# Kernel optimization log

Hardware: AMD Instinct MI355X
Metric: run time of the kernel (lower is better)

Reference implementation:

```python
import jax, jax.numpy as jnp
import numpy as np

N_M, N_C, D, H, E, EL = 200000, 50000, 128, 64, 1000000, 100000


def gat_conv(h_src, h_dst, W_src, W_dst, a_src, a_dst, b, src, dst, n_dst):
    # PyG GATConv (heads=1): project, per-edge attention logit, segment softmax over dst, weighted scatter-sum.
    hs = h_src @ W_src                      # [Ns, H]
    hd = h_dst @ W_dst                      # [Nd, H]
    al_s = hs @ a_src                       # [Ns]
    al_d = hd @ a_dst                       # [Nd]
    alpha = jax.nn.leaky_relu(al_s[src] + al_d[dst], 0.2)   # [E]
    m = jax.ops.segment_max(alpha, dst, num_segments=n_dst)
    m = jnp.where(jnp.isfinite(m), m, 0.0)
    e = jnp.exp(alpha - m[dst])
    denom = jax.ops.segment_sum(e, dst, num_segments=n_dst)
    w = e / jnp.maximum(denom[dst], 1e-16)
    out = jax.ops.segment_sum(w[:, None] * hs[src], dst, num_segments=n_dst)
    return out + b


def setup_inputs() -> dict:
    key = jax.random.key(0)
    ks = jax.random.split(key, 32)
    p = lambda k, s: (jax.random.normal(k, s, jnp.float32) * 0.1)
    inp = {
        'x_m': jax.random.normal(ks[0], (N_M, D), jnp.float32),
        'x_c': jax.random.normal(ks[1], (N_C, D), jnp.float32),
        'src_mc': jax.random.randint(ks[2], (E,), 0, N_M, jnp.int32),
        'dst_mc': jax.random.randint(ks[3], (E,), 0, N_C, jnp.int32),
        'src_cm': jax.random.randint(ks[4], (E,), 0, N_C, jnp.int32),
        'dst_cm': jax.random.randint(ks[5], (E,), 0, N_M, jnp.int32),
        'row': jax.random.randint(ks[6], (EL,), 0, N_M, jnp.int32),
        'col': jax.random.randint(ks[7], (EL,), 0, N_C, jnp.int32),
        'W1s_mc': p(ks[8], (D, H)), 'W1d_mc': p(ks[9], (D, H)),
        'a1s_mc': p(ks[10], (H,)), 'a1d_mc': p(ks[11], (H,)), 'b1_mc': p(ks[12], (H,)),
        'W1s_cm': p(ks[13], (D, H)), 'W1d_cm': p(ks[14], (D, H)),
        'a1s_cm': p(ks[15], (H,)), 'a1d_cm': p(ks[16], (H,)), 'b1_cm': p(ks[17], (H,)),
        'W2s_mc': p(ks[18], (H, H)), 'W2d_mc': p(ks[19], (H, H)),
        'a2s_mc': p(ks[20], (H,)), 'a2d_mc': p(ks[21], (H,)), 'b2_mc': p(ks[22], (H,)),
        'W2s_cm': p(ks[23], (H, H)), 'W2d_cm': p(ks[24], (H, H)),
        'a2s_cm': p(ks[25], (H,)), 'a2d_cm': p(ks[26], (H,)), 'b2_cm': p(ks[27], (H,)),
        'Wd1': p(ks[28], (2 * H, H)), 'bd1': p(ks[29], (H,)),
        'Wd2': p(ks[30], (H, 2)), 'bd2': p(ks[31], (2,)),
    }
    return inp


def reference(x_m, x_c, src_mc, dst_mc, src_cm, dst_cm, row, col,
              W1s_mc, W1d_mc, a1s_mc, a1d_mc, b1_mc,
              W1s_cm, W1d_cm, a1s_cm, a1d_cm, b1_cm,
              W2s_mc, W2d_mc, a2s_mc, a2d_mc, b2_mc,
              W2s_cm, W2d_cm, a2s_cm, a2d_cm, b2_cm,
              Wd1, bd1, Wd2, bd2):
    # Layer 1: materials receive only via concepts->materials edges; concepts via materials->concepts.
    z_c = jax.nn.relu(gat_conv(x_m, x_c, W1s_mc, W1d_mc, a1s_mc, a1d_mc, b1_mc, src_mc, dst_mc, N_C))
    z_m = jax.nn.relu(gat_conv(x_c, x_m, W1s_cm, W1d_cm, a1s_cm, a1d_cm, b1_cm, src_cm, dst_cm, N_M))
    # Layer 2 (no activation)
    z_c2 = gat_conv(z_m, z_c, W2s_mc, W2d_mc, a2s_mc, a2d_mc, b2_mc, src_mc, dst_mc, N_C)
    z_m2 = gat_conv(z_c, z_m, W2s_cm, W2d_cm, a2s_cm, a2d_cm, b2_cm, src_cm, dst_cm, N_M)
    # Edge decoder: gather-concat + 2-layer MLP (no activation between, per source)
    z = jnp.concatenate([z_m2[row], z_c2[col]], axis=-1)   # [EL, 2H]
    z = z @ Wd1 + bd1
    z = z @ Wd2 + bd2
    return z.reshape(-1)
```

## Files before the change

kernel.cpp:

```cpp
#include <hip/hip_runtime.h>
#include <hip/hip_fp16.h>
#include <cstdint>
#include <cstddef>

typedef _Float16 f16x8 __attribute__((ext_vector_type(8)));
typedef float f32x4 __attribute__((ext_vector_type(4)));

__device__ __forceinline__ float exp_am8(float a) {
    return __builtin_amdgcn_exp2f(fmaf(a, 1.442695040888963f, -11.541560327111707f));
}

__global__ void prep_all(
    const float* __restrict__ Wa0, const float* __restrict__ Wb0, _Float16* __restrict__ P0,
    const float* __restrict__ Wa1, const float* __restrict__ Wb1, _Float16* __restrict__ P1,
    const float* __restrict__ Wd1, const float* __restrict__ bd1,
    const float* __restrict__ Wd2, const float* __restrict__ bd2,
    const float* __restrict__ b2_cm, const float* __restrict__ b2_mc,
    const float* __restrict__ W2s_mc, const float* __restrict__ a2s_mc,
    const float* __restrict__ W2d_cm, const float* __restrict__ a2d_cm,
    const float* __restrict__ W2s_cm, const float* __restrict__ a2s_cm,
    const float* __restrict__ W2d_mc, const float* __restrict__ a2d_mc,
    float* __restrict__ Wc, float* __restrict__ bc, float* __restrict__ bq,
    float4* __restrict__ foldA, float4* __restrict__ foldB,
    int* __restrict__ bcnt_base) {
    __shared__ float WcS[256];
    int b = blockIdx.x;
    int t = threadIdx.x;
    if (b < 128) {
        const float* Wa; const float* Wb; _Float16* Wp; int lb;
        if (b < 64) { Wa = Wa0; Wb = Wb0; Wp = P0; lb = b; }
        else        { Wa = Wa1; Wb = Wb1; Wp = P1; lb = b - 64; }
        constexpr int K = 128;
        constexpr int NKB = K / 32;
        int i = lb * 256 + t;
        if (i >= 128 * K) return;
        int k = i >> 7, c = i & 127;
        float v = (c < 64) ? Wa[k * 64 + c] : Wb[k * 64 + (c - 64)];
        int ct = c >> 4, lr = c & 15, kb = k >> 5, lk = (k & 31) >> 3, e = k & 7;
        Wp[((ct * NKB + kb) * 64 + (lr + 16 * lk)) * 8 + e] = (_Float16)v;
    } else if (b == 128) {
        int k = t >> 1, c = t & 1;
        float s = 0.f;
        for (int j = 0; j < 64; ++j) s += Wd1[k * 64 + j] * Wd2[j * 2 + c];
        Wc[k * 2 + c] = s;
        WcS[k * 2 + c] = s;
        if (k == 0) {
            float bv = bd2[c];
            for (int j = 0; j < 64; ++j) bv += bd1[j] * Wd2[j * 2 + c];
            bc[c] = bv;
        }
        __syncthreads();
        if (t < 2) {
            float v = 0.f;
            for (int j = 0; j < 64; ++j) v += b2_cm[j] * WcS[j * 2 + t];
            bq[t] = v;
        } else if (t < 4) {
            int cc = t - 2;
            float v = 0.f;
            for (int j = 0; j < 64; ++j) v += b2_mc[j] * WcS[(64 + j) * 2 + cc];
            bq[t] = v;
        }
        if (t < 64) {
            int j = t;
            float fa = 0.f, fd = 0.f, qx = 0.f, qy = 0.f;
            for (int cc = 0; cc < 64; ++cc) {
                float ws = W2s_mc[j * 64 + cc];
                fa += ws * a2s_mc[cc];
                qx += ws * WcS[(64 + cc) * 2 + 0];
                qy += ws * WcS[(64 + cc) * 2 + 1];
                fd += W2d_cm[j * 64 + cc] * a2d_cm[cc];
            }
            foldA[j] = make_float4(fa, fd, qx, qy);
        } else if (t < 128) {
            int j = t - 64;
            float fa = 0.f, fd = 0.f, qx = 0.f, qy = 0.f;
            for (int cc = 0; cc < 64; ++cc) {
                float ws = W2s_cm[j * 64 + cc];
                fa += ws * a2s_cm[cc];
                qx += ws * WcS[cc * 2 + 0];
                qy += ws * WcS[cc * 2 + 1];
                fd += W2d_mc[j * 64 + cc] * a2d_mc[cc];
            }
            foldB[j] = make_float4(fa, fd, qx, qy);
        }
    } else {
        bcnt_base[t] = 0;
        bcnt_base[t + 256] = 0;
    }
}

#define XPAD 72

__device__ __forceinline__ void proj_body(const float* __restrict__ X, int N,
                                          const _Float16* __restrict__ Wp,
                                          const float* __restrict__ a0v,
                                          const float* __restrict__ a1v,
                                          __half* __restrict__ out0,
                                          float* __restrict__ al0,
                                          float* __restrict__ al1,
                                          char* smem, int blk) {
    constexpr int K = 128;
    _Float16* Xs = (_Float16*)smem;
    float* red0 = (float*)(smem + 128 * XPAD * 2);
    float* red1 = red0 + 128;
    int t = threadIdx.x;
    int wv = t >> 6, lane = t & 63, lr = lane & 15, lk = lane >> 4;
    int rt = blk * 128;
    int xrow = t >> 4;
    int xcp = t & 15;

    f16x8 wfr[4];
#pragma unroll
    for (int kbb = 0; kbb < 4; ++kbb)
        wfr[kbb] = ((const f16x8*)Wp)[(wv * 4 + kbb) * 64 + lane];

    if (t < 128) { red0[t] = 0.f; red1[t] = 0.f; }

    f32x4 acc[8];
#pragma unroll
    for (int i = 0; i < 8; ++i) acc[i] = f32x4{0.f, 0.f, 0.f, 0.f};

#pragma unroll
    for (int half = 0; half < 2; ++half) {
        __syncthreads();
#pragma unroll
        for (int pass = 0; pass < 4; ++pass) {
            int r = pass * 32 + xrow;
            int grow = rt + r;
            if (grow >= N) grow = N - 1;
            float4 v = *(const float4*)(X + (size_t)grow * K + half * 64 + xcp * 4);
            __half2 h01 = __floats2half2_rn(v.x, v.y);
            __half2 h23 = __floats2half2_rn(v.z, v.w);
            uint2 pk;
            pk.x = *(const unsigned int*)&h01;
            pk.y = *(const unsigned int*)&h23;
            *(uint2*)&Xs[r * XPAD + xcp * 4] = pk;
        }
        __syncthreads();
#pragma unroll
        for (int rt8 = 0; rt8 < 8; ++rt8) {
#pragma unroll
            for (int kb = 0; kb < 2; ++kb) {
                f16x8 bf = *(const f16x8*)&Xs[(rt8 * 16 + lr) * XPAD + kb * 32 + lk * 8];
                acc[rt8] = __builtin_amdgcn_mfma_f32_16x16x32_f16(
                    wfr[half * 2 + kb], bf, acc[rt8], 0, 0, 0);
            }
        }
    }

    bool is_s = wv < 4;
    float4 aq = is_s ? ((const float4*)a0v)[wv * 4 + lk]
                     : ((const float4*)a1v)[(wv - 4) * 4 + lk];
    float* red = is_s ? red0 : red1;
#pragma unroll
    for (int rt8 = 0; rt8 < 8; ++rt8) {
        f32x4 v = acc[rt8];
        float p = v[0] * aq.x + v[1] * aq.y + v[2] * aq.z + v[3] * aq.w;
        p += __shfl_xor(p, 16); p += __shfl_xor(p, 32);
        if (lane < 16) atomicAdd(&red[rt8 * 16 + lr], p);
        int row = rt + rt8 * 16 + lr;
        if (is_s && row < N) {
            __half2 h01 = __floats2half2_rn(v[0], v[1]);
            __half2 h23 = __floats2half2_rn(v[2], v[3]);
            uint2 pk;
            pk.x = *(const unsigned int*)&h01;
            pk.y = *(const unsigned int*)&h23;
            *(uint2*)(out0 + ((size_t)row << 6) + wv * 16 + lk * 4) = pk;
        }
    }
    __syncthreads();
    if (t < 128) {
        int row = rt + t;
        if (row < N) { al0[row] = red0[t]; al1[row] = red1[t]; }
    }
}

__global__ __launch_bounds__(512) void fused_proj_hist(
    const float* __restrict__ Xm, int Nm, const _Float16* __restrict__ WpA,
    const float* __restrict__ a0A, const float* __restrict__ a1A,
    __half* __restrict__ outA, float* __restrict__ al0A, float* __restrict__ al1A, int nbm,
    const float* __restrict__ Xc, int Nc, const _Float16* __restrict__ WpB,
    const float* __restrict__ a0B, const float* __restrict__ a1B,
    __half* __restrict__ outB, float* __restrict__ al0B, float* __restrict__ al1B, int nbc,
    const int* __restrict__ dmc, int* __restrict__ bcnt_mc, int shA,
    const int* __restrict__ dcm, int* __restrict__ bcnt_cm, int shB, int E, int nblk) {
    extern __shared__ __align__(16) char smem[];
    int b = blockIdx.x;
    if (b < nbm) {
        proj_body(Xm, Nm, WpA, a0A, a1A, outA, al0A, al1A, smem, b);
        return;
    }
    b -= nbm;
    if (b < nbc) {
        proj_body(Xc, Nc, WpB, a0B, a1B, outB, al0B, al1B, smem, b);
        return;
    }
    b -= nbc;
    int* h = (int*)smem;
    const int* dst; int* bcnt; int sh; int base;
    if (b < nblk) { dst = dmc; bcnt = bcnt_mc; sh = shA; base = b * 4096; }
    else { dst = dcm; bcnt = bcnt_cm; sh = shB; base = (b - nblk) * 4096; }
    int t = threadIdx.x;
    if (t < 256) h[t] = 0;
    __syncthreads();
#pragma unroll
    for (int j = 0; j < 8; ++j) {
        int i = base + j * 512 + t;
        if (i < E) atomicAdd(&h[dst[i] >> sh], 1);
    }
    __syncthreads();
    if (t < 256) {
        int c = h[t];
        if (c > 0) atomicAdd(&bcnt[t], c);
    }
}

__global__ void bucket_scan(const int* __restrict__ bcntA, int nbkA,
                            int* __restrict__ bbaseA, int* __restrict__ bcurA,
                            int* __restrict__ offA, int nA,
                            const int* __restrict__ bcntB, int nbkB,
                            int* __restrict__ bbaseB, int* __restrict__ bcurB,
                            int* __restrict__ offB, int nB, int E) {
    int t = threadIdx.x;
    if (t == 0) {
        int run = 0;
        for (int i = 0; i < nbkA; ++i) { bbaseA[i] = run; bcurA[i] = run; run += bcntA[i]; }
        bbaseA[nbkA] = run;
        offA[nA] = E;
    }
    if (t == 64) {
        int run = 0;
        for (int i = 0; i < nbkB; ++i) { bbaseB[i] = run; bcurB[i] = run; run += bcntB[i]; }
        bbaseB[nbkB] = run;
        offB[nB] = E;
    }
}

__global__ __launch_bounds__(256) void bucket_scatter(
    const int* __restrict__ srcA, const int* __restrict__ dstA,
    int* __restrict__ bcurA, unsigned* __restrict__ pairsA,
    const int* __restrict__ srcB, const int* __restrict__ dstB,
    int* __restrict__ bcurB, unsigned* __restrict__ pairsB,
    int E, int nblkA, int shA, int shB, int srcbits) {
    __shared__ int bcnt[256];
    __shared__ int bbase[256];
    const int* src; const int* dst; int* bcur; unsigned* pairs; int sh; int base;
    if ((int)blockIdx.x < nblkA) {
        src = srcA; dst = dstA; bcur = bcurA; pairs = pairsA; sh = shA;
        base = blockIdx.x * 4096;
    } else {
        src = srcB; dst = dstB; bcur = bcurB; pairs = pairsB; sh = shB;
        base = (blockIdx.x - nblkA) * 4096;
    }
    int t = threadIdx.x;
    int msk = (1 << sh) - 1;
    bcnt[t] = 0;
    __syncthreads();
    int sreg[16], dreg[16];
#pragma unroll
    for (int j = 0; j < 16; ++j) {
        int i = base + j * 256 + t;
        if (i < E) {
            sreg[j] = src[i];
            dreg[j] = dst[i];
            atomicAdd(&bcnt[dreg[j] >> sh], 1);
        } else {
            dreg[j] = -1;
        }
    }
    __syncthreads();
    {
        int c = bcnt[t];
        int g = (c > 0) ? atomicAdd(&bcur[t], c) : 0;
        bbase[t] = g;
        bcnt[t] = 0;
    }
    __syncthreads();
#pragma unroll
    for (int j = 0; j < 16; ++j) {
        if (dreg[j] >= 0) {
            int b = dreg[j] >> sh;
            int r = atomicAdd(&bcnt[b], 1);
            pairs[bbase[b] + r] = ((unsigned)(dreg[j] & msk) << srcbits) | (unsigned)sreg[j];
        }
    }
}

__global__ __launch_bounds__(256) void bucket_expand2(
    const unsigned* __restrict__ pairsA, const int* __restrict__ bbaseA, int nA,
    int* __restrict__ offA, int* __restrict__ csrA, int shA, int nbA,
    const unsigned* __restrict__ pairsB, const int* __restrict__ bbaseB, int nB,
    int* __restrict__ offB, int* __restrict__ csrB, int shB, int srcbits) {
    __shared__ int lcnt[1024];
    __shared__ int red[256];
    const unsigned* pairs; const int* bbase; int n; int* off; int* csr; int sh; int b;
    if ((int)blockIdx.x < nbA) {
        pairs = pairsA; bbase = bbaseA; n = nA; off = offA; csr = csrA; sh = shA;
        b = blockIdx.x;
    } else {
        pairs = pairsB; bbase = bbaseB; n = nB; off = offB; csr = csrB; sh = shB;
        b = blockIdx.x - nbA;
    }
    int dpb = 1 << sh;
    int d0 = b << sh;
    int t = threadIdx.x;
    unsigned smask = (1u << srcbits) - 1u;
    for (int dl = t; dl < dpb; dl += 256) lcnt[dl] = 0;
    __syncthreads();
    int pbeg = bbase[b], pend = bbase[b + 1];
    for (int i = pbeg + t; i < pend; i += 256)
        atomicAdd(&lcnt[pairs[i] >> srcbits], 1);
    __syncthreads();
    int per = (dpb + 255) >> 8;
    int i0 = t * per;
    int s = 0;
    for (int j = 0; j < per; ++j) {
        int dl = i0 + j;
        if (dl < dpb) s += lcnt[dl];
    }
    red[t] = s;
    __syncthreads();
    for (int st = 1; st < 256; st <<= 1) {
        int tmp = (t >= st) ? red[t - st] : 0;
        __syncthreads();
        red[t] += tmp;
        __syncthreads();
    }
    int run = pbeg + red[t] - s;
    for (int j = 0; j < per; ++j) {
        int dl = i0 + j;
        if (dl < dpb) {
            int c = lcnt[dl];
            if (d0 + dl < n) off[d0 + dl] = run;
            lcnt[dl] = run;
            run += c;
        }
    }
    __syncthreads();
    for (int i = pbeg + t; i < pend; i += 256) {
        unsigned p = pairs[i];
        int dl = (int)(p >> srcbits);
        int pos = atomicAdd(&lcnt[dl], 1);
        csr[pos] = (int)(p & smask);
    }
}

#define AGG_CAP 64
#define AGG_PAD 66

__global__ __launch_bounds__(256) void gat_aggregate9f(
    const int* __restrict__ off0, const int* __restrict__ csr0,
    const __half* __restrict__ hs0, const float* __restrict__ als0,
    const float* __restrict__ ald0, const float* __restrict__ bias0,
    const float4* __restrict__ fold0, float* __restrict__ als2_0,
    float* __restrict__ ald2_0, float2* __restrict__ q2_0, int n0,
    const int* __restrict__ off1, const int* __restrict__ csr1,
    const __half* __restrict__ hs1, const float* __restrict__ als1,
    const float* __restrict__ ald1, const float* __restrict__ bias1,
    const float4* __restrict__ fold1, float* __restrict__ als2_1,
    float* __restrict__ ald2_1, float2* __restrict__ q2_1, int n1,
    int nb0) {
    __shared__ uint2 wP[16][AGG_PAD];
    int t = threadIdx.x;
    int slot = t >> 4;
    int sub = t & 15;

    const int* off; const int* csr; const __half* hs; const float* als;
    const float* ald; const float* bias; const float4* fold;
    float* als2; float* ald2; float2* q2; int nd; int b;
    if (blockIdx.x < (unsigned)nb0) {
        b = blockIdx.x;
        off = off0; csr = csr0; hs = hs0; als = als0; ald = ald0; bias = bias0;
        fold = fold0; als2 = als2_0; ald2 = ald2_0; q2 = q2_0; nd = n0;
    } else {
        b = blockIdx.x - nb0;
        off = off1; csr = csr1; hs = hs1; als = als1; ald = ald1; bias = bias1;
        fold = fold1; als2 = als2_1; ald2 = ald2_1; q2 = q2_1; nd = n1;
    }
    int d = b * 16 + slot;
    bool active = d < nd;
    int beg = 0, deg = 0;
    float aldv = 0.f;
    if (active) {
        beg = off[d];
        deg = off[d + 1] - beg;
        aldv = ald[d];
    }
    float4 bl4 = ((const float4*)bias)[sub];
    uint2* WP = wP[slot];

    float sum = 0.f;
    for (int i = sub; i < deg; i += 16) {
        int s = csr[beg + i];
        float a = als[s] + aldv;
        a = (a >= 0.f) ? a : 0.2f * a;
        float w = exp_am8(a);
        sum += w;
        if (i < AGG_CAP) {
            __half hw = __float2half_rn(w);
            __half2 h2 = __half2half2(hw);
            WP[i] = make_uint2(*(const unsigned int*)&h2, (unsigned int)s);
        }
    }
    sum += __shfl_xor(sum, 1);
    sum += __shfl_xor(sum, 2);
    sum += __shfl_xor(sum, 4);
    sum += __shfl_xor(sum, 8);
    float inv = 1.f / fmaxf(sum, 1e-16f);

    int dc = deg < AGG_CAP ? deg : AGG_CAP;
    const uint2* hs4 = (const uint2*)hs;
    __half2 z = __floats2half2_rn(0.f, 0.f);
    __half2 aA = z, aB = z, aC = z, aD = z;
    int i = 0;
    for (; i + 8 <= dc; i += 8) {
        uint4 q0 = *(const uint4*)&WP[i];
        uint4 q1 = *(const uint4*)&WP[i + 2];
        uint4 q2r = *(const uint4*)&WP[i + 4];
        uint4 q3 = *(const uint4*)&WP[i + 6];
        uint2 v0 = hs4[(size_t)q0.y * 16 + sub];
        uint2 v1 = hs4[(size_t)q0.w * 16 + sub];
        uint2 v2 = hs4[(size_t)q1.y * 16 + sub];
        uint2 v3 = hs4[(size_t)q1.w * 16 + sub];
        uint2 v4 = hs4[(size_t)q2r.y * 16 + sub];
        uint2 v5 = hs4[(size_t)q2r.w * 16 + sub];
        uint2 v6 = hs4[(size_t)q3.y * 16 + sub];
        uint2 v7 = hs4[(size_t)q3.w * 16 + sub];
        aA = __hfma2(*(const __half2*)&q0.x, *(const __half2*)&v0.x, aA);
        aB = __hfma2(*(const __half2*)&q0.x, *(const __half2*)&v0.y, aB);
        aC = __hfma2(*(const __half2*)&q0.z, *(const __half2*)&v1.x, aC);
        aD = __hfma2(*(const __half2*)&q0.z, *(const __half2*)&v1.y, aD);
        aA = __hfma2(*(const __half2*)&q1.x, *(const __half2*)&v2.x, aA);
        aB = __hfma2(*(const __half2*)&q1.x, *(const __half2*)&v2.y, aB);
        aC = __hfma2(*(const __half2*)&q1.z, *(const __half2*)&v3.x, aC);
        aD = __hfma2(*(const __half2*)&q1.z, *(const __half2*)&v3.y, aD);
        aA = __hfma2(*(const __half2*)&q2r.x, *(const __half2*)&v4.x, aA);
        aB = __hfma2(*(const __half2*)&q2r.x, *(const __half2*)&v4.y, aB);
        aC = __hfma2(*(const __half2*)&q2r.z, *(const __half2*)&v5.x, aC);
        aD = __hfma2(*(const __half2*)&q2r.z, *(const __half2*)&v5.y, aD);
        aA = __hfma2(*(const __half2*)&q3.x, *(const __half2*)&v6.x, aA);
        aB = __hfma2(*(const __half2*)&q3.x, *(const __half2*)&v6.y, aB);
        aC = __hfma2(*(const __half2*)&q3.z, *(const __half2*)&v7.x, aC);
        aD = __hfma2(*(const __half2*)&q3.z, *(const __half2*)&v7.y, aD);
    }
    for (; i + 2 <= dc; i += 2) {
        uint4 q = *(const uint4*)&WP[i];
        uint2 v0 = hs4[(size_t)q.y * 16 + sub];
        uint2 v1 = hs4[(size_t)q.w * 16 + sub];
        aA = __hfma2(*(const __half2*)&q.x, *(const __half2*)&v0.x, aA);
        aB = __hfma2(*(const __half2*)&q.x, *(const __half2*)&v0.y, aB);
        aC = __hfma2(*(const __half2*)&q.z, *(const __half2*)&v1.x, aC);
        aD = __hfma2(*(const __half2*)&q.z, *(const __half2*)&v1.y, aD);
    }
    if (i < dc) {
        uint2 u = WP[i];
        uint2 v = hs4[(size_t)u.y * 16 + sub];
        aA = __hfma2(*(const __half2*)&u.x, *(const __half2*)&v.x, aA);
        aB = __hfma2(*(const __half2*)&u.x, *(const __half2*)&v.y, aB);
    }
    for (int j = AGG_CAP; j < deg; ++j) {
        int s = csr[beg + j];
        float a = als[s] + aldv;
        a = (a >= 0.f) ? a : 0.2f * a;
        __half hw = __float2half_rn(exp_am8(a));
        __half2 w2 = __half2half2(hw);
        uint2 v = hs4[(size_t)s * 16 + sub];
        aA = __hfma2(w2, *(const __half2*)&v.x, aA);
        aB = __hfma2(w2, *(const __half2*)&v.y, aB);
    }
    float2 fA = __half22float2(aA);
    float2 fB = __half22float2(aB);
    float2 fC = __half22float2(aC);
    float2 fD = __half22float2(aD);
    float o0 = (fA.x + fC.x) * inv + bl4.x;
    float o1 = (fA.y + fC.y) * inv + bl4.y;
    float o2 = (fB.x + fD.x) * inv + bl4.z;
    float o3 = (fB.y + fD.y) * inv + bl4.w;
    if (deg == 0) { o0 = bl4.x; o1 = bl4.y; o2 = bl4.z; o3 = bl4.w; }
    o0 = fmaxf(o0, 0.f); o1 = fmaxf(o1, 0.f);
    o2 = fmaxf(o2, 0.f); o3 = fmaxf(o3, 0.f);

    float4 f0 = fold[4 * sub + 0];
    float4 f1 = fold[4 * sub + 1];
    float4 f2 = fold[4 * sub + 2];
    float4 f3 = fold[4 * sub + 3];
    float a0 = o0 * f0.x + o1 * f1.x + o2 * f2.x + o3 * f3.x;
    float a1 = o0 * f0.y + o1 * f1.y + o2 * f2.y + o3 * f3.y;
    float a2 = o0 * f0.z + o1 * f1.z + o2 * f2.z + o3 * f3.z;
    float a3 = o0 * f0.w + o1 * f1.w + o2 * f2.w + o3 * f3.w;
#pragma unroll
    for (int o = 1; o < 16; o <<= 1) {
        a0 += __shfl_xor(a0, o);
        a1 += __shfl_xor(a1, o);
        a2 += __shfl_xor(a2, o);
        a3 += __shfl_xor(a3, o);
    }
    if (active && sub == 0) {
        als2[d] = a0;
        ald2[d] = a1;
        q2[d] = make_float2(a2, a3);
    }
}

__global__ __launch_bounds__(256) void gat_aggregate10p(
    const int* __restrict__ off0, const int* __restrict__ csr0,
    const float2* __restrict__ q0, const float* __restrict__ als0,
    const float* __restrict__ ald0, const float2* __restrict__ bqp,
    float2* __restrict__ out0, int n0,
    const int* __restrict__ off1, const int* __restrict__ csr1,
    const float2* __restrict__ q1, const float* __restrict__ als1,
    const float* __restrict__ ald1,
    float2* __restrict__ out1, int n1,
    int nb0) {
    const int* off; const int* csr; const float2* qt; const float* als;
    const float* ald; float2 bq; float2* outp; int nd; int b;
    if (blockIdx.x < (unsigned)nb0) {
        b = blockIdx.x;
        off = off0; csr = csr0; qt = q0; als = als0; ald = ald0; bq = bqp[1];
        outp = out0; nd = n0;
    } else {
        b = blockIdx.x - nb0;
        off = off1; csr = csr1; qt = q1; als = als1; ald = ald1; bq = bqp[0];
        outp = out1; nd = n1;
    }
    int d = b * 256 + threadIdx.x;
    if (d >= nd) return;
    int beg = off[d], end = off[d + 1];
    float aldv = ald[d];
    float sum = 0.f, ax = 0.f, ay = 0.f;
    int i = beg;
    for (; i + 2 <= end; i += 2) {
        int s0 = csr[i], s1 = csr[i + 1];
        float a0 = als[s0] + aldv;
        float a1 = als[s1] + aldv;
        float2 v0 = qt[s0];
        float2 v1 = qt[s1];
        a0 = (a0 >= 0.f) ? a0 : 0.2f * a0;
        a1 = (a1 >= 0.f) ? a1 : 0.2f * a1;
        float w0 = exp_am8(a0);
        float w1 = exp_am8(a1);
        sum += w0 + w1;
        ax = fmaf(w0, v0.x, ax); ay = fmaf(w0, v0.y, ay);
        ax = fmaf(w1, v1.x, ax); ay = fmaf(w1, v1.y, ay);
    }
    if (i < end) {
        int s = csr[i];
        float a = als[s] + aldv;
        a = (a >= 0.f) ? a : 0.2f * a;
        float w = exp_am8(a);
        float2 v = qt[s];
        sum += w;
        ax = fmaf(w, v.x, ax); ay = fmaf(w, v.y, ay);
    }
    float inv = 1.f / fmaxf(sum, 1e-16f);
    outp[d] = make_float2(ax * inv + bq.x, ay * inv + bq.y);
}

__global__ __launch_bounds__(256) void decoder4_kernel(const int* __restrict__ row,
                                                       const int* __restrict__ col,
                                                       const float2* __restrict__ pm,
                                                       const float2* __restrict__ pc,
                                                       const float* __restrict__ bc,
                                                       float* __restrict__ out, int EL) {
    int e = blockIdx.x * 256 + threadIdx.x;
    if (e >= EL) return;
    float2 a = pm[row[e]];
    float2 b = pc[col[e]];
    *(float2*)(out + 2 * (size_t)e) = make_float2(a.x + b.x + bc[0], a.y + b.y + bc[1]);
}

extern "C" void kernel_launch(void* const* d_in, const int* in_sizes, int n_in,
                              void* d_out, int out_size, void* d_ws, size_t ws_size,
                              hipStream_t stream) {
    const int D = 128;
    const float* x_m    = (const float*)d_in[0];
    const float* x_c    = (const float*)d_in[1];
    const int*   src_mc = (const int*)d_in[2];
    const int*   dst_mc = (const int*)d_in[3];
    const int*   src_cm = (const int*)d_in[4];
    const int*   dst_cm = (const int*)d_in[5];
    const int*   rowi   = (const int*)d_in[6];
    const int*   coli   = (const int*)d_in[7];
    const float* W1s_mc = (const float*)d_in[8];
    const float* W1d_mc = (const float*)d_in[9];
    const float* a1s_mc = (const float*)d_in[10];
    const float* a1d_mc = (const float*)d_in[11];
    const float* b1_mc  = (const float*)d_in[12];
    const float* W1s_cm = (const float*)d_in[13];
    const float* W1d_cm = (const float*)d_in[14];
    const float* a1s_cm = (const float*)d_in[15];
    const float* a1d_cm = (const float*)d_in[16];
    const float* b1_cm  = (const float*)d_in[17];
    const float* W2s_mc = (const float*)d_in[18];
    const float* W2d_mc = (const float*)d_in[19];
    const float* a2s_mc = (const float*)d_in[20];
    const float* a2d_mc = (const float*)d_in[21];
    const float* b2_mc  = (const float*)d_in[22];
    const float* W2s_cm = (const float*)d_in[23];
    const float* W2d_cm = (const float*)d_in[24];
    const float* a2s_cm = (const float*)d_in[25];
    const float* a2d_cm = (const float*)d_in[26];
    const float* b2_cm  = (const float*)d_in[27];
    const float* Wd1    = (const float*)d_in[28];
    const float* bd1    = (const float*)d_in[29];
    const float* Wd2    = (const float*)d_in[30];
    const float* bd2    = (const float*)d_in[31];

    const int N_M = in_sizes[0] / D;
    const int N_C = in_sizes[1] / D;
    const int E   = in_sizes[2];
    const int EL  = in_sizes[6];
    float* out = (float*)d_out;

    uint8_t* base = (uint8_t*)d_ws;
    size_t off = 0;
    auto carve = [&](size_t bytes) -> void* {
        void* p = base + off;
        off += (bytes + 255) & ~(size_t)255;
        return p;
    };
    __half* hsA_h = (__half*)carve((size_t)N_M * 64 * 2);
    __half* hsB_h = (__half*)carve((size_t)N_C * 64 * 2);
    float2* qA    = (float2*)carve((size_t)N_M * 8);
    float2* qB    = (float2*)carve((size_t)N_C * 8);
    float2* pm_m  = (float2*)carve((size_t)N_M * 8);
    float2* pm_c  = (float2*)carve((size_t)N_C * 8);
    float* als_mc = (float*)carve((size_t)N_M * 4);
    float* ald_cm = (float*)carve((size_t)N_M * 4);
    float* als_cm = (float*)carve((size_t)N_C * 4);
    float* ald_mc = (float*)carve((size_t)N_C * 4);
    float* als2_mc = (float*)carve((size_t)N_M * 4);
    float* ald2_cm = (float*)carve((size_t)N_M * 4);
    float* als2_cm = (float*)carve((size_t)N_C * 4);
    float* ald2_mc = (float*)carve((size_t)N_C * 4);
    int* off_mc = (int*)carve((size_t)(N_C + 1) * 4);
    int* off_cm = (int*)carve((size_t)(N_M + 1) * 4);
    int* csr_mc = (int*)carve((size_t)E * 4);
    int* csr_cm = (int*)carve((size_t)E * 4);
    unsigned* pairs_mc = (unsigned*)carve((size_t)E * 4);
    unsigned* pairs_cm = (unsigned*)carve((size_t)E * 4);
    int* bcnt_base = (int*)carve(512 * 4);
    int* bcnt_mc = bcnt_base;
    int* bcnt_cm = bcnt_base + 256;
    int* bbase_mc = (int*)carve(257 * 4);
    int* bbase_cm = (int*)carve(257 * 4);
    int* bcur_mc = (int*)carve(256 * 4);
    int* bcur_cm = (int*)carve(256 * 4);
    _Float16* wp1A = (_Float16*)carve(128 * 128 * 2);
    _Float16* wp1B = (_Float16*)carve(128 * 128 * 2);
    float* Wc = (float*)carve(256 * 4);
    float* bc = (float*)carve(256);
    float* bq = (float*)carve(256);
    float2* bq2 = (float2*)bq;
    float4* foldA = (float4*)carve(64 * 16);
    float4* foldB = (float4*)carve(64 * 16);

    int shA = 0; while (((N_C + (1 << shA) - 1) >> shA) > 256) shA++;
    int shB = 0; while (((N_M + (1 << shB) - 1) >> shB) > 256) shB++;
    int nbkA = (N_C + (1 << shA) - 1) >> shA;
    int nbkB = (N_M + (1 << shB) - 1) >> shB;
    int maxN = N_M > N_C ? N_M : N_C;
    int srcbits = 1; while ((1 << srcbits) < maxN) srcbits++;

    prep_all<<<130, 256, 0, stream>>>(W1s_mc, W1d_cm, wp1A, W1s_cm, W1d_mc, wp1B,
                                      Wd1, bd1, Wd2, bd2, b2_cm, b2_mc,
                                      W2s_mc, a2s_mc, W2d_cm, a2d_cm,
                                      W2s_cm, a2s_cm, W2d_mc, a2d_mc,
                                      Wc, bc, bq, foldA, foldB, bcnt_base);

    int nbm = (N_M + 127) / 128;
    int nbc = (N_C + 127) / 128;
    int nblk = (E + 4095) / 4096;
    size_t smem_bytes = (size_t)128 * XPAD * 2 + 256 * 4;
    fused_proj_hist<<<nbm + nbc + 2 * nblk, 512, smem_bytes, stream>>>(
        x_m, N_M, wp1A, a1s_mc, a1d_cm, hsA_h, als_mc, ald_cm, nbm,
        x_c, N_C, wp1B, a1s_cm, a1d_mc, hsB_h, als_cm, ald_mc, nbc,
        dst_mc, bcnt_mc, shA, dst_cm, bcnt_cm, shB, E, nblk);

    bucket_scan<<<1, 128, 0, stream>>>(bcnt_mc, nbkA, bbase_mc, bcur_mc, off_mc, N_C,
                                       bcnt_cm, nbkB, bbase_cm, bcur_cm, off_cm, N_M, E);
    bucket_scatter<<<2 * nblk, 256, 0, stream>>>(
        src_mc, dst_mc, bcur_mc, pairs_mc,
        src_cm, dst_cm, bcur_cm, pairs_cm, E, nblk, shA, shB, srcbits);
    bucket_expand2<<<nbkA + nbkB, 256, 0, stream>>>(
        pairs_mc, bbase_mc, N_C, off_mc, csr_mc, shA, nbkA,
        pairs_cm, bbase_cm, N_M, off_cm, csr_cm, shB, srcbits);

    int nb_c16 = (N_C + 15) / 16;
    int nb_m16 = (N_M + 15) / 16;

    gat_aggregate9f<<<nb_c16 + nb_m16, 256, 0, stream>>>(
        off_mc, csr_mc, hsA_h, als_mc, ald_mc, b1_mc, foldB, als2_cm, ald2_mc, qB, N_C,
        off_cm, csr_cm, hsB_h, als_cm, ald_cm, b1_cm, foldA, als2_mc, ald2_cm, qA, N_M,
        nb_c16);

    int nb_c256 = (N_C + 255) / 256;
    int nb_m256 = (N_M + 255) / 256;
    gat_aggregate10p<<<nb_c256 + nb_m256, 256, 0, stream>>>(
        off_mc, csr_mc, qA, als2_mc, ald2_mc, bq2, pm_c, N_C,
        off_cm, csr_cm, qB, als2_cm, ald2_cm, pm_m, N_M, nb_c256);

    decoder4_kernel<<<(EL + 255) / 256, 256, 0, stream>>>(rowi, coli, pm_m, pm_c, bc, out, EL);
}
```

Before: 197.4 us.

## Process four row tiles per projection block and stage full-K tile in LDS

```diff
diff --git a/kernel.cpp b/kernel.cpp
--- a/kernel.cpp
+++ b/kernel.cpp
@@ -89,7 +89,7 @@
     }
 }
 
-#define XPAD 72
+#define XP 136
 
 __device__ __forceinline__ void proj_body(const float* __restrict__ X, int N,
                                           const _Float16* __restrict__ Wp,
@@ -98,14 +98,13 @@
                                           __half* __restrict__ out0,
                                           float* __restrict__ al0,
                                           float* __restrict__ al1,
-                                          char* smem, int blk) {
+                                          char* smem, int blk, int ntile) {
     constexpr int K = 128;
     _Float16* Xs = (_Float16*)smem;
-    float* red0 = (float*)(smem + 128 * XPAD * 2);
+    float* red0 = (float*)(smem + 128 * XP * 2);
     float* red1 = red0 + 128;
     int t = threadIdx.x;
     int wv = t >> 6, lane = t & 63, lr = lane & 15, lk = lane >> 4;
-    int rt = blk * 128;
     int xrow = t >> 4;
     int xcp = t & 15;
 
@@ -113,65 +112,75 @@
 #pragma unroll
     for (int kbb = 0; kbb < 4; ++kbb)
         wfr[kbb] = ((const f16x8*)Wp)[(wv * 4 + kbb) * 64 + lane];
-
-    if (t < 128) { red0[t] = 0.f; red1[t] = 0.f; }
-
-    f32x4 acc[8];
-#pragma unroll
-    for (int i = 0; i < 8; ++i) acc[i] = f32x4{0.f, 0.f, 0.f, 0.f};
-
-#pragma unroll
-    for (int half = 0; half < 2; ++half) {
-        __syncthreads();
-#pragma unroll
-        for (int pass = 0; pass < 4; ++pass) {
-            int r = pass * 32 + xrow;
-            int grow = rt + r;
-            if (grow >= N) grow = N - 1;
-            float4 v = *(const float4*)(X + (size_t)grow * K + half * 64 + xcp * 4);
-            __half2 h01 = __floats2half2_rn(v.x, v.y);
-            __half2 h23 = __floats2half2_rn(v.z, v.w);
-            uint2 pk;
-            pk.x = *(const unsigned int*)&h01;
-            pk.y = *(const unsigned int*)&h23;
-            *(uint2*)&Xs[r * XPAD + xcp * 4] = pk;
-        }
-        __syncthreads();
-#pragma unroll
-        for (int rt8 = 0; rt8 < 8; ++rt8) {
-#pragma unroll
-            for (int kb = 0; kb < 2; ++kb) {
-                f16x8 bf = *(const f16x8*)&Xs[(rt8 * 16 + lr) * XPAD + kb * 32 + lk * 8];
-                acc[rt8] = __builtin_amdgcn_mfma_f32_16x16x32_f16(
-                    wfr[half * 2 + kb], bf, acc[rt8], 0, 0, 0);
-            }
-        }
-    }
 
     bool is_s = wv < 4;
     float4 aq = is_s ? ((const float4*)a0v)[wv * 4 + lk]
                      : ((const float4*)a1v)[(wv - 4) * 4 + lk];
     float* red = is_s ? red0 : red1;
-#pragma unroll
-    for (int rt8 = 0; rt8 < 8; ++rt8) {
-        f32x4 v = acc[rt8];
-        float p = v[0] * aq.x + v[1] * aq.y + v[2] * aq.z + v[3] * aq.w;
-        p += __shfl_xor(p, 16); p += __shfl_xor(p, 32);
-        if (lane < 16) atomicAdd(&red[rt8 * 16 + lr], p);
-        int row = rt + rt8 * 16 + lr;
-        if (is_s && row < N) {
-            __half2 h01 = __floats2half2_rn(v[0], v[1]);
-            __half2 h23 = __floats2half2_rn(v[2], v[3]);
+
+    for (int tile = 0; tile < ntile; ++tile) {
+        int rt = (blk * ntile + tile) * 128;
+        if (rt >= N) break;
+        float4 v[8];
+#pragma unroll
+        for (int p = 0; p < 4; ++p) {
+            int grow = rt + p * 32 + xrow;
+            if (grow >= N) grow = N - 1;
+            const float* rp = X + (size_t)grow * K + xcp * 4;
+            v[p] = *(const float4*)rp;
+            v[4 + p] = *(const float4*)(rp + 64);
+        }
+        __syncthreads();
+#pragma unroll
+        for (int p = 0; p < 4; ++p) {
+            int r = p * 32 + xrow;
+            __half2 h01 = __floats2half2_rn(v[p].x, v[p].y);
+            __half2 h23 = __floats2half2_rn(v[p].z, v[p].w);
             uint2 pk;
             pk.x = *(const unsigned int*)&h01;
             pk.y = *(const unsigned int*)&h23;
-            *(uint2*)(out0 + ((size_t)row << 6) + wv * 16 + lk * 4) = pk;
-        }
-    }
-    __syncthreads();
-    if (t < 128) {
-        int row = rt + t;
-        if (row < N) { al0[row] = red0[t]; al1[row] = red1[t]; }
+            *(uint2*)&Xs[r * XP + xcp * 4] = pk;
+            h01 = __floats2half2_rn(v[4 + p].x, v[4 + p].y);
+            h23 = __floats2half2_rn(v[4 + p].z, v[4 + p].w);
+            pk.x = *(const unsigned int*)&h01;
+            pk.y = *(const unsigned int*)&h23;
+            *(uint2*)&Xs[r * XP + 64 + xcp * 4] = pk;
+        }
+        if (t < 128) { red0[t] = 0.f; red1[t] = 0.f; }
+        __syncthreads();
+        f32x4 acc[8];
+#pragma unroll
+        for (int i = 0; i < 8; ++i) acc[i] = f32x4{0.f, 0.f, 0.f, 0.f};
+#pragma unroll
+        for (int rt8 = 0; rt8 < 8; ++rt8) {
+#pragma unroll
+            for (int kbb = 0; kbb < 4; ++kbb) {
+                f16x8 bf = *(const f16x8*)&Xs[(rt8 * 16 + lr) * XP + kbb * 32 + lk * 8];
+                acc[rt8] = __builtin_amdgcn_mfma_f32_16x16x32_f16(
+                    wfr[kbb], bf, acc[rt8], 0, 0, 0);
+            }
+        }
+#pragma unroll
+        for (int rt8 = 0; rt8 < 8; ++rt8) {
+            f32x4 vv = acc[rt8];
+            float p = vv[0] * aq.x + vv[1] * aq.y + vv[2] * aq.z + vv[3] * aq.w;
+            p += __shfl_xor(p, 16); p += __shfl_xor(p, 32);
+            if (lane < 16) atomicAdd(&red[rt8 * 16 + lr], p);
+            int row = rt + rt8 * 16 + lr;
+            if (is_s && row < N) {
+                __half2 h01 = __floats2half2_rn(vv[0], vv[1]);
+                __half2 h23 = __floats2half2_rn(vv[2], vv[3]);
+                uint2 pk;
+                pk.x = *(const unsigned int*)&h01;
+                pk.y = *(const unsigned int*)&h23;
+                *(uint2*)(out0 + ((size_t)row << 6) + wv * 16 + lk * 4) = pk;
+            }
+        }
+        __syncthreads();
+        if (t < 128) {
+            int row = rt + t;
+            if (row < N) { al0[row] = red0[t]; al1[row] = red1[t]; }
+        }
     }
 }
 
@@ -183,16 +192,17 @@
     const float* __restrict__ a0B, const float* __restrict__ a1B,
     __half* __restrict__ outB, float* __restrict__ al0B, float* __restrict__ al1B, int nbc,
     const int* __restrict__ dmc, int* __restrict__ bcnt_mc, int shA,
-    const int* __restrict__ dcm, int* __restrict__ bcnt_cm, int shB, int E, int nblk) {
+    const int* __restrict__ dcm, int* __restrict__ bcnt_cm, int shB, int E, int nblk,
+    int ntile) {
     extern __shared__ __align__(16) char smem[];
     int b = blockIdx.x;
     if (b < nbm) {
-        proj_body(Xm, Nm, WpA, a0A, a1A, outA, al0A, al1A, smem, b);
+        proj_body(Xm, Nm, WpA, a0A, a1A, outA, al0A, al1A, smem, b, ntile);
         return;
     }
     b -= nbm;
     if (b < nbc) {
-        proj_body(Xc, Nc, WpB, a0B, a1B, outB, al0B, al1B, smem, b);
+        proj_body(Xc, Nc, WpB, a0B, a1B, outB, al0B, al1B, smem, b, ntile);
         return;
     }
     b -= nbc;
@@ -668,14 +678,15 @@
                                       W2s_cm, a2s_cm, W2d_mc, a2d_mc,
                                       Wc, bc, bq, foldA, foldB, bcnt_base);
 
-    int nbm = (N_M + 127) / 128;
-    int nbc = (N_C + 127) / 128;
+    const int NTILE = 4;
+    int nbm = (N_M + 128 * NTILE - 1) / (128 * NTILE);
+    int nbc = (N_C + 128 * NTILE - 1) / (128 * NTILE);
     int nblk = (E + 4095) / 4096;
-    size_t smem_bytes = (size_t)128 * XPAD * 2 + 256 * 4;
+    size_t smem_bytes = (size_t)128 * XP * 2 + 256 * 4;
     fused_proj_hist<<<nbm + nbc + 2 * nblk, 512, smem_bytes, stream>>>(
         x_m, N_M, wp1A, a1s_mc, a1d_cm, hsA_h, als_mc, ald_cm, nbm,
         x_c, N_C, wp1B, a1s_cm, a1d_mc, hsB_h, als_cm, ald_mc, nbc,
-        dst_mc, bcnt_mc, shA, dst_cm, bcnt_cm, shB, E, nblk);
+        dst_mc, bcnt_mc, shA, dst_cm, bcnt_cm, shB, E, nblk, NTILE);
 
     bucket_scan<<<1, 128, 0, stream>>>(bcnt_mc, nbkA, bbase_mc, bcur_mc, off_mc, N_C,
                                        bcnt_cm, nbkB, bbase_cm, bcur_cm, off_cm, N_M, E);
```

New measurement: 193.3 us. 2.1% less time.
